# Kernel optimization log

Hardware: AMD Instinct MI355X
Metric: run time of the kernel (lower is better)

Reference implementation:

```python
import jax, jax.numpy as jnp
import numpy as np

# Haar (db1) decomposition filters, pywt convention
_S = 1.0 / np.sqrt(2.0)
# dec_lo = [s, s], dec_hi = [-s, s]. Each scalar input v becomes signal [v, 0]
# (zero-pad to 2**dwt_level = 2). The single valid DWT coeff (mode='zero') is
#   cA = v * dec_lo[1] = v * s ;  cD = v * dec_hi[1] = v * s
CA_COEF = np.float32(_S)   # dec_lo[1]
CD_COEF = np.float32(_S)   # dec_hi[1]

B, N, F, OUT = 8, 20000, 256, 256
WAVELET_FULL_LEN = 2  # len(cA) + len(cD) for level-1 db1 on length-2 signal


def setup_inputs() -> dict:
    key = jax.random.key(0)
    kx, kw, kb, kwo, kbo = jax.random.split(key, 5)
    x = jax.random.normal(kx, (B, N, F), dtype=jnp.float32)
    # per-feature nn.Linear(wavelet_full_len, 1) stacked: weight [F, 2], bias [F]
    lim_nl = 1.0 / np.sqrt(WAVELET_FULL_LEN)
    W_nl = jax.random.uniform(kw, (F, WAVELET_FULL_LEN), jnp.float32, -lim_nl, lim_nl)
    b_nl = jax.random.uniform(kb, (F,), jnp.float32, -lim_nl, lim_nl)
    # linear_out: [out_dim, feat_dim] torch layout, bias [out_dim]
    lim_o = 1.0 / np.sqrt(F)
    W_out = jax.random.uniform(kwo, (OUT, F), jnp.float32, -lim_o, lim_o)
    b_out = jax.random.uniform(kbo, (OUT,), jnp.float32, -lim_o, lim_o)
    return {"x": x, "W_nl": W_nl, "b_nl": b_nl, "W_out": W_out, "b_out": b_out}


def reference(x, W_nl, b_nl, W_out, b_out):
    # Batched wavelet features: for each scalar, coeffs are [cA, cD] = [s*v, s*v]
    # feat_wave: [B, N, F, 2]
    feat_wave = jnp.stack([x * CA_COEF, x * CD_COEF], axis=-1)
    # Per-feature Linear(2, 1), batched over the feature dim
    agg_nl = jnp.einsum("bnfk,fk->bnf", feat_wave, W_nl) + b_nl  # [B, N, F]
    # Output linear (dropout is identity in eval)
    out = jnp.einsum("bnf,of->bno", agg_nl, W_out) + b_out  # [B, N, OUT]
    return out
```

## Files before the change

kernel.cpp:

```cpp
#include <hip/hip_runtime.h>

typedef __bf16 bf16x8 __attribute__((ext_vector_type(8)));
typedef float f32x4 __attribute__((ext_vector_type(4)));
typedef unsigned short ushort8 __attribute__((ext_vector_type(8)));

__device__ __forceinline__ unsigned short f2b(float f) {
    unsigned int u = __float_as_uint(f);
    return (unsigned short)((u + 0x7fffu + ((u >> 16) & 1u)) >> 16);
}

__global__ __launch_bounds__(256) void wk_prep(
    const float* __restrict__ Wnl, const float* __restrict__ bnl,
    const float* __restrict__ Wout, const float* __restrict__ bout,
    unsigned short* __restrict__ wfrag, float* __restrict__ wbias) {
    int b = blockIdx.x, tid = threadIdx.x;
    if (b < 256) {
        int t = b * 256 + tid;
        int j = t & 7;
        int lane = (t >> 3) & 63;
        int ks = (t >> 9) & 7;
        int ct = t >> 12;
        int f = ks * 32 + ((lane >> 4) << 3) + j;
        int o = ct * 16 + (lane & 15);
        float c = 0.70710678f * (Wnl[2 * f] + Wnl[2 * f + 1]);
        wfrag[t] = f2b(c * Wout[o * 256 + f]);
    } else {
        int o = tid;
        float s = 0.f;
        #pragma unroll 8
        for (int f = 0; f < 256; ++f) s += bnl[f] * Wout[o * 256 + f];
        wbias[o] = bout[o] + s;
    }
}

__global__ __launch_bounds__(512, 4) void wk_main(
    const float* __restrict__ x, const unsigned short* __restrict__ wfrag,
    const float* __restrict__ wbias, float* __restrict__ out) {
    const int tid  = threadIdx.x;
    const int lane = tid & 63;
    const int w    = tid >> 6;
    const int m    = lane & 15;
    const int quad = lane >> 4;
    const int r0   = blockIdx.x * 128 + w * 16;

    __shared__ bf16x8 Wlds[4096];

    {
        int4* dst = (int4*)Wlds;
        const int4* src = (const int4*)wfrag;
        #pragma unroll
        for (int i = 0; i < 8; ++i) dst[tid + i * 512] = src[tid + i * 512];
    }

    const float4* xv = (const float4*)(x + (size_t)(r0 + m) * 256);
    bf16x8 afr[8];
    #pragma unroll
    for (int c = 0; c < 2; ++c) {
        float4 u[4], v[4];
        #pragma unroll
        for (int q = 0; q < 4; ++q) {
            int ks = c * 4 + q;
            u[q] = xv[ks * 8 + quad * 2];
            v[q] = xv[ks * 8 + quad * 2 + 1];
        }
        #pragma unroll
        for (int q = 0; q < 4; ++q) {
            ushort8 s;
            s[0] = f2b(u[q].x); s[1] = f2b(u[q].y);
            s[2] = f2b(u[q].z); s[3] = f2b(u[q].w);
            s[4] = f2b(v[q].x); s[5] = f2b(v[q].y);
            s[6] = f2b(v[q].z); s[7] = f2b(v[q].w);
            afr[c * 4 + q] = __builtin_bit_cast(bf16x8, s);
        }
    }

    __syncthreads();

    #pragma unroll
    for (int h = 0; h < 2; ++h) {
        if (h == 1) {
            __syncthreads();
            int4* dst = (int4*)Wlds;
            const int4* src = (const int4*)(wfrag + 32768);
            #pragma unroll
            for (int i = 0; i < 8; ++i) dst[tid + i * 512] = src[tid + i * 512];
            __syncthreads();
        }
        #pragma unroll
        for (int ct = 0; ct < 8; ++ct) {
            float b = wbias[h * 128 + ct * 16 + m];
            f32x4 acc = {b, b, b, b};
            #pragma unroll
            for (int ks = 0; ks < 8; ++ks) {
                acc = __builtin_amdgcn_mfma_f32_16x16x32_bf16(
                    afr[ks], Wlds[(ct * 8 + ks) * 64 + lane], acc, 0, 0, 0);
            }
            size_t base = (size_t)(r0 + quad * 4) * 256 + h * 128 + ct * 16 + m;
            out[base]       = acc[0];
            out[base + 256] = acc[1];
            out[base + 512] = acc[2];
            out[base + 768] = acc[3];
        }
    }
}

extern "C" void kernel_launch(void* const* d_in, const int* in_sizes, int n_in,
                              void* d_out, int out_size, void* d_ws, size_t ws_size,
                              hipStream_t stream) {
    const float* x    = (const float*)d_in[0];
    const float* Wnl  = (const float*)d_in[1];
    const float* bnl  = (const float*)d_in[2];
    const float* Wout = (const float*)d_in[3];
    const float* bout = (const float*)d_in[4];

    unsigned short* wfrag = (unsigned short*)d_ws;
    float* wbias = (float*)((char*)d_ws + 131072);

    wk_prep<<<257, 256, 0, stream>>>(Wnl, bnl, Wout, bout, wfrag, wbias);
    wk_main<<<1250, 512, 0, stream>>>(x, wfrag, wbias, (float*)d_out);
}
```

Measured before the change: 300.3 us.

## Persistent waves with full weight in LDS, prefetch next tile, transposed MFMA stores

Rewrites the main kernel as a persistent grid of 256 blocks of 12 waves. Each wave walks a contiguous range of 16-row tiles and prefetches the next tile's x into registers while computing the current one. The full 256x256 bf16 weight (128KB) and the fused bias are loaded into LDS once per block, which removes the two-phase weight reload and its extra barriers. MFMA operands are swapped so each lane holds 4 consecutive output columns, allowing vector nontemporal float4 stores. The risks are higher LDS use and register pressure from the 16 float4 prefetch buffers, which limit occupancy.

```diff
diff --git a/kernel.cpp b/kernel.cpp
--- a/kernel.cpp
+++ b/kernel.cpp
@@ -26,14 +26,19 @@
         wfrag[t] = f2b(c * Wout[o * 256 + f]);
     } else {
         int o = tid;
+        const float4* wr = (const float4*)(Wout + o * 256);
+        const float4* bn = (const float4*)bnl;
         float s = 0.f;
-        #pragma unroll 8
-        for (int f = 0; f < 256; ++f) s += bnl[f] * Wout[o * 256 + f];
+        #pragma unroll 4
+        for (int i = 0; i < 64; ++i) {
+            float4 a = bn[i], b4 = wr[i];
+            s += a.x * b4.x + a.y * b4.y + a.z * b4.z + a.w * b4.w;
+        }
         wbias[o] = bout[o] + s;
     }
 }
 
-__global__ __launch_bounds__(512, 4) void wk_main(
+__global__ __launch_bounds__(768, 3) void wk_main(
     const float* __restrict__ x, const unsigned short* __restrict__ wfrag,
     const float* __restrict__ wbias, float* __restrict__ out) {
     const int tid  = threadIdx.x;
@@ -41,66 +46,62 @@
     const int w    = tid >> 6;
     const int m    = lane & 15;
     const int quad = lane >> 4;
-    const int r0   = blockIdx.x * 128 + w * 16;
 
-    __shared__ bf16x8 Wlds[4096];
+    __shared__ bf16x8 Wlds[8192];
+    __shared__ f32x4  blds[64];
 
+    const int gw = blockIdx.x * 12 + w;
+    int t        = (gw * 10000) / 3072;
+    const int t1 = ((gw + 1) * 10000) / 3072;
+
+    float4 buf[16];
+    {
+        const float4* xv = (const float4*)(x + ((size_t)t * 16 + m) * 256);
+        #pragma unroll
+        for (int ks = 0; ks < 8; ++ks) {
+            buf[2 * ks]     = xv[ks * 8 + quad * 2];
+            buf[2 * ks + 1] = xv[ks * 8 + quad * 2 + 1];
+        }
+    }
     {
         int4* dst = (int4*)Wlds;
         const int4* src = (const int4*)wfrag;
-        #pragma unroll
-        for (int i = 0; i < 8; ++i) dst[tid + i * 512] = src[tid + i * 512];
+        for (int i = tid; i < 8192; i += 768) dst[i] = src[i];
+        if (tid < 64) blds[tid] = ((const f32x4*)wbias)[tid];
     }
-
-    const float4* xv = (const float4*)(x + (size_t)(r0 + m) * 256);
-    bf16x8 afr[8];
-    #pragma unroll
-    for (int c = 0; c < 2; ++c) {
-        float4 u[4], v[4];
-        #pragma unroll
-        for (int q = 0; q < 4; ++q) {
-            int ks = c * 4 + q;
-            u[q] = xv[ks * 8 + quad * 2];
-            v[q] = xv[ks * 8 + quad * 2 + 1];
-        }
-        #pragma unroll
-        for (int q = 0; q < 4; ++q) {
-            ushort8 s;
-            s[0] = f2b(u[q].x); s[1] = f2b(u[q].y);
-            s[2] = f2b(u[q].z); s[3] = f2b(u[q].w);
-            s[4] = f2b(v[q].x); s[5] = f2b(v[q].y);
-            s[6] = f2b(v[q].z); s[7] = f2b(v[q].w);
-            afr[c * 4 + q] = __builtin_bit_cast(bf16x8, s);
-        }
-    }
-
     __syncthreads();
 
-    #pragma unroll
-    for (int h = 0; h < 2; ++h) {
-        if (h == 1) {
-            __syncthreads();
-            int4* dst = (int4*)Wlds;
-            const int4* src = (const int4*)(wfrag + 32768);
-            #pragma unroll
-            for (int i = 0; i < 8; ++i) dst[tid + i * 512] = src[tid + i * 512];
-            __syncthreads();
+    while (true) {
+        bf16x8 afr[8];
+        #pragma unroll
+        for (int ks = 0; ks < 8; ++ks) {
+            float4 u = buf[2 * ks], v = buf[2 * ks + 1];
+            ushort8 s;
+            s[0] = f2b(u.x); s[1] = f2b(u.y); s[2] = f2b(u.z); s[3] = f2b(u.w);
+            s[4] = f2b(v.x); s[5] = f2b(v.y); s[6] = f2b(v.z); s[7] = f2b(v.w);
+            afr[ks] = __builtin_bit_cast(bf16x8, s);
         }
-        #pragma unroll
-        for (int ct = 0; ct < 8; ++ct) {
-            float b = wbias[h * 128 + ct * 16 + m];
-            f32x4 acc = {b, b, b, b};
+        const int tn = t + 1;
+        if (tn < t1) {
+            const float4* xv = (const float4*)(x + ((size_t)tn * 16 + m) * 256);
             #pragma unroll
             for (int ks = 0; ks < 8; ++ks) {
+                buf[2 * ks]     = xv[ks * 8 + quad * 2];
+                buf[2 * ks + 1] = xv[ks * 8 + quad * 2 + 1];
+            }
+        }
+        float* outp = out + ((size_t)t * 16 + m) * 256 + quad * 4;
+        #pragma unroll
+        for (int ct = 0; ct < 16; ++ct) {
+            f32x4 acc = blds[ct * 4 + quad];
+            #pragma unroll
+            for (int ks = 0; ks < 8; ++ks)
                 acc = __builtin_amdgcn_mfma_f32_16x16x32_bf16(
-                    afr[ks], Wlds[(ct * 8 + ks) * 64 + lane], acc, 0, 0, 0);
-            }
-            size_t base = (size_t)(r0 + quad * 4) * 256 + h * 128 + ct * 16 + m;
-            out[base]       = acc[0];
-            out[base + 256] = acc[1];
-            out[base + 512] = acc[2];
-            out[base + 768] = acc[3];
+                    Wlds[(ct * 8 + ks) * 64 + lane], afr[ks], acc, 0, 0, 0);
+            __builtin_nontemporal_store(acc, (f32x4*)(outp + ct * 16));
         }
+        if (tn >= t1) break;
+        t = tn;
     }
 }
 
@@ -117,5 +118,5 @@
     float* wbias = (float*)((char*)d_ws + 131072);
 
     wk_prep<<<257, 256, 0, stream>>>(Wnl, bnl, Wout, bout, wfrag, wbias);
-    wk_main<<<1250, 512, 0, stream>>>(x, wfrag, wbias, (float*)d_out);
+    wk_main<<<256, 768, 0, stream>>>(x, wfrag, wbias, (float*)d_out);
 }
```

New measurement: 744.2 us. +147.8%, slower.
